# Performance work log

Measured on AMD Instinct MI355X. Metric: run time of the kernel, lower is better.

The kernel has to match this reference:

```python
import jax, jax.numpy as jnp
import numpy as np

GRID_LO = 32
GRID_HI = 128
NF = 4          # n_features
K = 9           # num_neighbors
NUM_CLASSES = 36
BS = 128
P_LO = GRID_LO * GRID_LO   # 1024
P_HI = GRID_HI * GRID_HI   # 16384


def _knn_neighbor_indices():
    """Replicates cKDTree(lo_coords).query(hi_coords, k=K)[1]: lo grid has
    spacing ratio=grid_hi//grid_lo, hi grid spacing 1; neighbors sorted by
    distance (stable sort -> ties broken by lower linear index)."""
    ratio = GRID_HI // GRID_LO
    lo = np.stack(np.meshgrid(np.arange(GRID_LO) * ratio,
                              np.arange(GRID_LO) * ratio, indexing='ij'),
                  axis=-1).reshape(-1, 2).astype(np.float64)   # (P_LO, 2)
    hi = np.stack(np.meshgrid(np.arange(GRID_HI),
                              np.arange(GRID_HI), indexing='ij'),
                  axis=-1).reshape(-1, 2).astype(np.float64)   # (P_HI, 2)
    d2 = ((hi[:, None, :] - lo[None, :, :]) ** 2).sum(-1)      # (P_HI, P_LO)
    idx = np.argsort(d2, axis=1, kind='stable')[:, :K]          # (P_HI, K)
    return jnp.asarray(idx, dtype=jnp.int32)


def setup_inputs() -> dict:
    key = jax.random.key(0)
    k1, k2, k3, k4, k5 = jax.random.split(key, 5)
    x = jax.random.normal(k1, (BS, NF * P_LO), dtype=jnp.float32)
    cls_ids = jax.random.randint(k2, (BS,), 0, NUM_CLASSES)
    neighbor_indices = _knn_neighbor_indices()                  # (P_HI, K)
    weight_map = jax.random.normal(k3, (NUM_CLASSES, NF, P_HI, K), dtype=jnp.float32) * 0.05
    bias_low = jax.random.normal(k4, (NUM_CLASSES, NF, P_LO), dtype=jnp.float32) * 0.05
    bias_high = jax.random.normal(k5, (NUM_CLASSES, NF, P_HI), dtype=jnp.float32) * 0.05
    return {"x": x, "cls_ids": cls_ids, "neighbor_indices": neighbor_indices,
            "weight_map": weight_map, "bias_low": bias_low, "bias_high": bias_high}


def reference(x, cls_ids, neighbor_indices, weight_map, bias_low, bias_high):
    # x: (BS, NF*P_LO) -> (BS, NF, P_LO)
    y_low = x.reshape(x.shape[0], NF, P_LO)
    y_low_db = y_low - bias_low[cls_ids]                        # (BS, NF, P_LO)
    # gather k=9 lo-res neighbors for every hi-res pixel (all features at once)
    neigh = y_low_db[:, :, neighbor_indices]                    # (BS, NF, P_HI, K)
    weights = weight_map[cls_ids]                               # (BS, NF, P_HI, K)
    out = jnp.einsum('bfpk,bfpk->bfp', neigh, weights)          # weighted sum over k
    out = out + bias_high[cls_ids]                              # (BS, NF, P_HI)
    return out.reshape(x.shape[0], NF, GRID_HI, GRID_HI)
```

## Files before the change

### kernel.cpp

```cpp
#include <hip/hip_runtime.h>

#define BS      128
#define NF      4
#define NC      36
#define P_LO    1024
#define P_HI    16384
#define KNN     9
#define THREADS 256
#define TILE_P  256
#define NTILES  (P_HI / TILE_P)
#define LIST_OFF 64
#define SCHED_OFF 36

__global__ __launch_bounds__(128) void build_lists_kernel(
    const int* __restrict__ cls_ids, int* __restrict__ ws)
{
    __shared__ int cnt[NC];
    __shared__ int pk[9];
    const int t = threadIdx.x;
    if (t < NC) cnt[t] = 0;
    if (t >= 64 && t < 73) pk[t - 64] = 0;
    __syncthreads();
    if (t < BS) {
        int c = cls_ids[t];
        int pos = atomicAdd(&cnt[c], 1);
        ws[LIST_OFF + c * BS + pos] = t;
    }
    __syncthreads();
    if (t < NC) {
        int ct = cnt[t];
        ws[t] = ct;
        int r = 0;
        for (int j = 0; j < NC; ++j) {
            int cj = cnt[j];
            r += (cj > ct) || (cj == ct && j < t);
        }
        atomicOr(&pk[r >> 2], t << ((r & 3) << 3));
    }
    __syncthreads();
    if (t < 9) ws[SCHED_OFF + t] = pk[t];
}

__device__ __forceinline__ void async_cp16(const void* g, void* l) {
    __builtin_amdgcn_global_load_lds(
        (const __attribute__((address_space(1))) void*)g,
        (__attribute__((address_space(3))) void*)l, 16, 0, 0);
}

__global__ __launch_bounds__(THREADS) void rect_up_kernel(
    const float* __restrict__ x,
    const int*   __restrict__ ws,
    const int*   __restrict__ nbr,
    const float* __restrict__ wmap,
    const float* __restrict__ blo,
    const float* __restrict__ bhi,
    float*       __restrict__ out)
{
    __shared__ __align__(16) float ybuf[2][4][P_LO];

    const int tile = blockIdx.x & (NTILES - 1);
    const int rank = blockIdx.x >> 6;
    const int cls  = (ws[SCHED_OFF + (rank >> 2)] >> ((rank & 3) << 3)) & 0xFF;
    const int n_b  = ws[cls];
    if (n_b == 0) return;

    const int tid = threadIdx.x;
    const int p   = tile * TILE_P + tid;
    const int* list = ws + LIST_OFF + cls * BS;

    const int i00 = list[0];
    const int i01 = (1 < n_b) ? list[1] : i00;
    const int i02 = (2 < n_b) ? list[2] : i00;
    const int i03 = (3 < n_b) ? list[3] : i00;

    int id0 = i00, id1 = i01, id2 = i02, id3 = i03;

    async_cp16(x + (size_t)(id0 * NF + 0) * P_LO + tid * 4, &ybuf[0][0][tid * 4]);
    async_cp16(x + (size_t)(id1 * NF + 0) * P_LO + tid * 4, &ybuf[0][1][tid * 4]);
    async_cp16(x + (size_t)(id2 * NF + 0) * P_LO + tid * 4, &ybuf[0][2][tid * 4]);
    async_cp16(x + (size_t)(id3 * NF + 0) * P_LO + tid * 4, &ybuf[0][3][tid * 4]);

    float w[KNN]; int nb[KNN];
    {
        const float* wr = wmap + ((size_t)(cls * NF + 0) * P_HI + p) * KNN;
        const int*   ir = nbr + (size_t)p * KNN;
        #pragma unroll
        for (int k = 0; k < KNN; ++k) { w[k] = wr[k]; nb[k] = ir[k]; }
    }
    float bhc = bhi[(size_t)(cls * NF + 0) * P_HI + p];
    {
        const float* blp = blo + (size_t)(cls * NF + 0) * P_LO;
        #pragma unroll
        for (int k = 0; k < KNN; ++k) bhc = fmaf(-w[k], blp[nb[k]], bhc);
    }

    asm volatile("s_waitcnt vmcnt(0) lgkmcnt(0)" ::: "memory");
    __builtin_amdgcn_s_barrier();

    const int R = (n_b + 3) >> 2;
    int cur = 0;

    float wn[KNN], blg[KNN], bhn;

    for (int f = 0; f < NF; ++f) {
        for (int r = 0; r < R; ++r) {
            const bool fb   = (r == R - 1) && (f < NF - 1);
            const bool last = (r == R - 1) && (f == NF - 1);

            int n0 = id0, n1 = id1, n2 = id2, n3 = id3, nf = f;
            if (fb) { n0 = i00; n1 = i01; n2 = i02; n3 = i03; nf = f + 1; }
            else if (r + 1 < R) {
                const int s = 4 * (r + 1);
                n0 = list[s];
                n1 = (s + 1 < n_b) ? list[s + 1] : n0;
                n2 = (s + 2 < n_b) ? list[s + 2] : n0;
                n3 = (s + 3 < n_b) ? list[s + 3] : n0;
            }

            if (!last) {
                float* dst = &ybuf[cur ^ 1][0][0];
                async_cp16(x + (size_t)(n0 * NF + nf) * P_LO + tid * 4, dst + 0 * P_LO + tid * 4);
                async_cp16(x + (size_t)(n1 * NF + nf) * P_LO + tid * 4, dst + 1 * P_LO + tid * 4);
                async_cp16(x + (size_t)(n2 * NF + nf) * P_LO + tid * 4, dst + 2 * P_LO + tid * 4);
                async_cp16(x + (size_t)(n3 * NF + nf) * P_LO + tid * 4, dst + 3 * P_LO + tid * 4);
                __builtin_amdgcn_sched_barrier(0);
            }

            if (fb) {
                const float* wrn = wmap + ((size_t)(cls * NF + nf) * P_HI + p) * KNN;
                #pragma unroll
                for (int k = 0; k < KNN; ++k) wn[k] = wrn[k];
                bhn = bhi[(size_t)(cls * NF + nf) * P_HI + p];
                const float* blpn = blo + (size_t)(cls * NF + nf) * P_LO;
                #pragma unroll
                for (int k = 0; k < KNN; ++k) blg[k] = blpn[nb[k]];
            }

            const float* yb = &ybuf[cur][0][0];
            float a0 = 0.f, a1 = 0.f, a2 = 0.f, a3 = 0.f;
            #pragma unroll
            for (int k = 0; k < KNN; ++k) {
                const int o = nb[k];
                a0 = fmaf(w[k], yb[o], a0);
                a1 = fmaf(w[k], yb[o + P_LO], a1);
                a2 = fmaf(w[k], yb[o + 2 * P_LO], a2);
                a3 = fmaf(w[k], yb[o + 3 * P_LO], a3);
            }

            out[(size_t)(id0 * NF + f) * P_HI + p] = a0 + bhc;
            out[(size_t)(id1 * NF + f) * P_HI + p] = a1 + bhc;
            out[(size_t)(id2 * NF + f) * P_HI + p] = a2 + bhc;
            out[(size_t)(id3 * NF + f) * P_HI + p] = a3 + bhc;

            if (fb) {
                float t = bhn;
                #pragma unroll
                for (int k = 0; k < KNN; ++k) t = fmaf(-wn[k], blg[k], t);
                bhn = t;
            }

            if (!last) {
                asm volatile("s_waitcnt vmcnt(4) lgkmcnt(0)" ::: "memory");
                __builtin_amdgcn_s_barrier();
                cur ^= 1;
                id0 = n0; id1 = n1; id2 = n2; id3 = n3;
                if (fb) {
                    #pragma unroll
                    for (int k = 0; k < KNN; ++k) w[k] = wn[k];
                    bhc = bhn;
                }
            }
        }
    }
}

extern "C" void kernel_launch(void* const* d_in, const int* in_sizes, int n_in,
                              void* d_out, int out_size, void* d_ws, size_t ws_size,
                              hipStream_t stream) {
    const float* x    = (const float*)d_in[0];
    const int*   cls  = (const int*)d_in[1];
    const int*   nbr  = (const int*)d_in[2];
    const float* wmap = (const float*)d_in[3];
    const float* blo  = (const float*)d_in[4];
    const float* bhi  = (const float*)d_in[5];
    float*       out  = (float*)d_out;
    int*         wsl  = (int*)d_ws;

    build_lists_kernel<<<1, 128, 0, stream>>>(cls, wsl);
    rect_up_kernel<<<NC * NTILES, THREADS, 0, stream>>>(
        x, wsl, nbr, wmap, blo, bhi, out);
}
```

Baseline: 166.6 us.

## Load only needed low-res slice per tile with register prefetch pipeline

Each block now loads only a 192-element window of the low-res image, the rows its hi-res tile can touch, instead of the full 1024-pixel feature map per sample. The data goes into LDS interleaved by sample, so one float4 LDS read serves all four samples. Async global-to-LDS copies are replaced by a three-deep register prefetch pipeline that writes each stage into the double-buffered LDS. This cuts global traffic for x and the LDS footprint, at the cost of more registers and synchronous LDS stores each phase.

```diff
diff --git a/kernel.cpp b/kernel.cpp
--- a/kernel.cpp
+++ b/kernel.cpp
@@ -11,6 +11,7 @@
 #define NTILES  (P_HI / TILE_P)
 #define LIST_OFF 64
 #define SCHED_OFF 36
+#define SLICE   192
 
 __global__ __launch_bounds__(128) void build_lists_kernel(
     const int* __restrict__ cls_ids, int* __restrict__ ws)
@@ -41,12 +42,6 @@
     if (t < 9) ws[SCHED_OFF + t] = pk[t];
 }
 
-__device__ __forceinline__ void async_cp16(const void* g, void* l) {
-    __builtin_amdgcn_global_load_lds(
-        (const __attribute__((address_space(1))) void*)g,
-        (__attribute__((address_space(3))) void*)l, 16, 0, 0);
-}
-
 __global__ __launch_bounds__(THREADS) void rect_up_kernel(
     const float* __restrict__ x,
     const int*   __restrict__ ws,
@@ -56,7 +51,7 @@
     const float* __restrict__ bhi,
     float*       __restrict__ out)
 {
-    __shared__ __align__(16) float ybuf[2][4][P_LO];
+    __shared__ __align__(16) float ybuf[2][SLICE][4];
 
     const int tile = blockIdx.x & (NTILES - 1);
     const int rank = blockIdx.x >> 6;
@@ -66,112 +61,125 @@
 
     const int tid = threadIdx.x;
     const int p   = tile * TILE_P + tid;
+    const int m   = tile >> 1;
+    const int base32 = (min(max(m - 2, 0), 26)) << 5;
+    const int s   = tid >> 6;
+    const int qq  = tid & 63;
+
     const int* list = ws + LIST_OFF + cls * BS;
-
-    const int i00 = list[0];
-    const int i01 = (1 < n_b) ? list[1] : i00;
-    const int i02 = (2 < n_b) ? list[2] : i00;
-    const int i03 = (3 < n_b) ? list[3] : i00;
-
-    int id0 = i00, id1 = i01, id2 = i02, id3 = i03;
-
-    async_cp16(x + (size_t)(id0 * NF + 0) * P_LO + tid * 4, &ybuf[0][0][tid * 4]);
-    async_cp16(x + (size_t)(id1 * NF + 0) * P_LO + tid * 4, &ybuf[0][1][tid * 4]);
-    async_cp16(x + (size_t)(id2 * NF + 0) * P_LO + tid * 4, &ybuf[0][2][tid * 4]);
-    async_cp16(x + (size_t)(id3 * NF + 0) * P_LO + tid * 4, &ybuf[0][3][tid * 4]);
-
-    float w[KNN]; int nb[KNN];
-    {
-        const float* wr = wmap + ((size_t)(cls * NF + 0) * P_HI + p) * KNN;
-        const int*   ir = nbr + (size_t)p * KNN;
-        #pragma unroll
-        for (int k = 0; k < KNN; ++k) { w[k] = wr[k]; nb[k] = ir[k]; }
-    }
-    float bhc = bhi[(size_t)(cls * NF + 0) * P_HI + p];
-    {
-        const float* blp = blo + (size_t)(cls * NF + 0) * P_LO;
-        #pragma unroll
-        for (int k = 0; k < KNN; ++k) bhc = fmaf(-w[k], blp[nb[k]], bhc);
-    }
-
-    asm volatile("s_waitcnt vmcnt(0) lgkmcnt(0)" ::: "memory");
+    const int R  = (n_b + 3) >> 2;
+    const int NP = NF * R;
+
+#define WAVE_ID(rr) ((4 * (rr) + s < n_b) ? list[4 * (rr) + s] : list[4 * (rr)])
+#define LOAD_XP(dst, ff, rr) {                                               \
+        const int id_ = WAVE_ID(rr);                                         \
+        const float* xp_ = x + ((size_t)id_ * NF + (ff)) * P_LO + base32 + qq; \
+        dst[0] = xp_[0]; dst[1] = xp_[64]; dst[2] = xp_[128]; }
+
+    int nbl[KNN];
+    {
+        const int* ir = nbr + (size_t)p * KNN;
+        #pragma unroll
+        for (int k = 0; k < KNN; ++k) nbl[k] = ir[k] - base32;
+    }
+    float w_[KNN];
+    {
+        const float* wr = wmap + ((size_t)cls * NF * P_HI + p) * KNN;
+        #pragma unroll
+        for (int k = 0; k < KNN; ++k) w_[k] = wr[k];
+    }
+    float bhc;
+    {
+        float t = bhi[(size_t)cls * NF * P_HI + p];
+        const float* blp = blo + (size_t)cls * NF * P_LO + base32;
+        #pragma unroll
+        for (int k = 0; k < KNN; ++k) t = fmaf(-w_[k], blp[nbl[k]], t);
+        bhc = t;
+    }
+
+    float xp1[3], xp2[3], xp3[3];
+    {
+        float x0[3];
+        LOAD_XP(x0, 0, 0);
+        LOAD_XP(xp1, 1 / R, 1 % R);
+        LOAD_XP(xp2, 2 / R, 2 % R);
+        LOAD_XP(xp3, 3 / R, 3 % R);
+        #pragma unroll
+        for (int t = 0; t < 3; ++t) ybuf[0][qq + 64 * t][s] = x0[t];
+    }
+    asm volatile("s_waitcnt lgkmcnt(0)" ::: "memory");
     __builtin_amdgcn_s_barrier();
 
-    const int R = (n_b + 3) >> 2;
-    int cur = 0;
-
-    float wn[KNN], blg[KNN], bhn;
-
-    for (int f = 0; f < NF; ++f) {
-        for (int r = 0; r < R; ++r) {
-            const bool fb   = (r == R - 1) && (f < NF - 1);
-            const bool last = (r == R - 1) && (f == NF - 1);
-
-            int n0 = id0, n1 = id1, n2 = id2, n3 = id3, nf = f;
-            if (fb) { n0 = i00; n1 = i01; n2 = i02; n3 = i03; nf = f + 1; }
-            else if (r + 1 < R) {
-                const int s = 4 * (r + 1);
-                n0 = list[s];
-                n1 = (s + 1 < n_b) ? list[s + 1] : n0;
-                n2 = (s + 2 < n_b) ? list[s + 2] : n0;
-                n3 = (s + 3 < n_b) ? list[s + 3] : n0;
-            }
-
-            if (!last) {
-                float* dst = &ybuf[cur ^ 1][0][0];
-                async_cp16(x + (size_t)(n0 * NF + nf) * P_LO + tid * 4, dst + 0 * P_LO + tid * 4);
-                async_cp16(x + (size_t)(n1 * NF + nf) * P_LO + tid * 4, dst + 1 * P_LO + tid * 4);
-                async_cp16(x + (size_t)(n2 * NF + nf) * P_LO + tid * 4, dst + 2 * P_LO + tid * 4);
-                async_cp16(x + (size_t)(n3 * NF + nf) * P_LO + tid * 4, dst + 3 * P_LO + tid * 4);
-                __builtin_amdgcn_sched_barrier(0);
-            }
-
-            if (fb) {
-                const float* wrn = wmap + ((size_t)(cls * NF + nf) * P_HI + p) * KNN;
-                #pragma unroll
-                for (int k = 0; k < KNN; ++k) wn[k] = wrn[k];
-                bhn = bhi[(size_t)(cls * NF + nf) * P_HI + p];
-                const float* blpn = blo + (size_t)(cls * NF + nf) * P_LO;
-                #pragma unroll
-                for (int k = 0; k < KNN; ++k) blg[k] = blpn[nb[k]];
-            }
-
-            const float* yb = &ybuf[cur][0][0];
-            float a0 = 0.f, a1 = 0.f, a2 = 0.f, a3 = 0.f;
-            #pragma unroll
-            for (int k = 0; k < KNN; ++k) {
-                const int o = nb[k];
-                a0 = fmaf(w[k], yb[o], a0);
-                a1 = fmaf(w[k], yb[o + P_LO], a1);
-                a2 = fmaf(w[k], yb[o + 2 * P_LO], a2);
-                a3 = fmaf(w[k], yb[o + 3 * P_LO], a3);
-            }
-
-            out[(size_t)(id0 * NF + f) * P_HI + p] = a0 + bhc;
-            out[(size_t)(id1 * NF + f) * P_HI + p] = a1 + bhc;
-            out[(size_t)(id2 * NF + f) * P_HI + p] = a2 + bhc;
-            out[(size_t)(id3 * NF + f) * P_HI + p] = a3 + bhc;
-
-            if (fb) {
-                float t = bhn;
-                #pragma unroll
-                for (int k = 0; k < KNN; ++k) t = fmaf(-wn[k], blg[k], t);
-                bhn = t;
-            }
-
-            if (!last) {
-                asm volatile("s_waitcnt vmcnt(4) lgkmcnt(0)" ::: "memory");
-                __builtin_amdgcn_s_barrier();
-                cur ^= 1;
-                id0 = n0; id1 = n1; id2 = n2; id3 = n3;
-                if (fb) {
-                    #pragma unroll
-                    for (int k = 0; k < KNN; ++k) w[k] = wn[k];
-                    bhc = bhn;
-                }
-            }
-        }
-    }
+    int pb = 0, f = 0, r = 0;
+    int f3 = 4 / R, r3 = 4 % R;
+    float wn[KNN], bhn = 0.f;
+
+    for (int ph = 0; ph < NP; ++ph) {
+        const int s0  = 4 * r;
+        const int id0 = list[s0];
+        const int id1 = (s0 + 1 < n_b) ? list[s0 + 1] : id0;
+        const int id2 = (s0 + 2 < n_b) ? list[s0 + 2] : id0;
+        const int id3 = (s0 + 3 < n_b) ? list[s0 + 3] : id0;
+
+        if (ph + 1 < NP) {
+            #pragma unroll
+            for (int t = 0; t < 3; ++t) ybuf[pb ^ 1][qq + 64 * t][s] = xp1[t];
+        }
+
+        #pragma unroll
+        for (int t = 0; t < 3; ++t) { xp1[t] = xp2[t]; xp2[t] = xp3[t]; }
+        if (f3 < NF) LOAD_XP(xp3, f3, r3);
+
+        float blgn[KNN];
+        const bool fb = (r == 0) && (f + 1 < NF);
+        if (fb) {
+            const float* wrn = wmap + ((size_t)(cls * NF + f + 1) * P_HI + p) * KNN;
+            #pragma unroll
+            for (int k = 0; k < KNN; ++k) wn[k] = wrn[k];
+            const float* blpn = blo + (size_t)(cls * NF + f + 1) * P_LO + base32;
+            #pragma unroll
+            for (int k = 0; k < KNN; ++k) blgn[k] = blpn[nbl[k]];
+            bhn = bhi[(size_t)(cls * NF + f + 1) * P_HI + p];
+        }
+
+        const float* yb = &ybuf[pb][0][0];
+        float a0 = 0.f, a1 = 0.f, a2 = 0.f, a3 = 0.f;
+        #pragma unroll
+        for (int k = 0; k < KNN; ++k) {
+            const float4 yv = *(const float4*)(yb + 4 * nbl[k]);
+            a0 = fmaf(w_[k], yv.x, a0);
+            a1 = fmaf(w_[k], yv.y, a1);
+            a2 = fmaf(w_[k], yv.z, a2);
+            a3 = fmaf(w_[k], yv.w, a3);
+        }
+
+        out[((size_t)id0 * NF + f) * P_HI + p] = a0 + bhc;
+        out[((size_t)id1 * NF + f) * P_HI + p] = a1 + bhc;
+        out[((size_t)id2 * NF + f) * P_HI + p] = a2 + bhc;
+        out[((size_t)id3 * NF + f) * P_HI + p] = a3 + bhc;
+
+        if (fb) {
+            float t = bhn;
+            #pragma unroll
+            for (int k = 0; k < KNN; ++k) t = fmaf(-wn[k], blgn[k], t);
+            bhn = t;
+        }
+
+        if (ph + 1 < NP) {
+            asm volatile("s_waitcnt lgkmcnt(0)" ::: "memory");
+            __builtin_amdgcn_s_barrier();
+        }
+        pb ^= 1;
+        if (++r == R) {
+            r = 0; ++f;
+            #pragma unroll
+            for (int k = 0; k < KNN; ++k) w_[k] = wn[k];
+            bhc = bhn;
+        }
+        if (++r3 == R) { r3 = 0; ++f3; }
+    }
+#undef LOAD_XP
+#undef WAVE_ID
 }
 
 extern "C" void kernel_launch(void* const* d_in, const int* in_sizes, int n_in,
```

After: 163.5 us. No clear change (-1.9%).
